# Performance work log

Measured on AMD Instinct MI355X. Metric: run time of the kernel, lower is better.

The kernel has to match this reference:

```python
import jax, jax.numpy as jnp
import numpy as np

B, N, E, H = 256, 256, 256, 512


def setup_inputs() -> dict:
    key = jax.random.key(0)
    ks = jax.random.split(key, 8)
    sH = 1.0 / np.sqrt(H)  # torch default init scale for LSTMCell / Linear fan_in
    sE = 1.0 / np.sqrt(E)
    return {
        "encoder_output": jax.random.normal(ks[0], (B, N, E), dtype=jnp.float32),
        "W_ih": jax.random.uniform(ks[1], (4 * H, E), jnp.float32, -sH, sH),
        "W_hh": jax.random.uniform(ks[2], (4 * H, H), jnp.float32, -sH, sH),
        "b_ih": jax.random.uniform(ks[3], (4 * H,), jnp.float32, -sH, sH),
        "b_hh": jax.random.uniform(ks[4], (4 * H,), jnp.float32, -sH, sH),
        "W_q": jax.random.uniform(ks[5], (H, H), jnp.float32, -sH, sH),
        "W_k": jax.random.uniform(ks[6], (H, E), jnp.float32, -sE, sE),
        "v": jax.random.uniform(ks[7], (H,), jnp.float32, -sH, sH),
        "max_steps": 256,
    }


def reference(encoder_output, W_ih, W_hh, b_ih, b_hh, W_q, W_k, v, max_steps):
    b, n, e = encoder_output.shape
    h_dim = W_hh.shape[1]
    # W_k(encoder_output) is loop-invariant -> hoist (same math as original)
    k_enc = jnp.einsum("bne,he->bnh", encoder_output, W_k)  # (B, N, H)
    keys = jax.random.split(jax.random.key(42), max_steps)
    batch_idx = jnp.arange(b)

    def step(carry, key):
        h, c, start, visited_mask = carry
        # torch LSTMCell: gates in i, f, g, o order
        gates = start @ W_ih.T + b_ih + h @ W_hh.T + b_hh  # (B, 4H)
        i, f, g, o = jnp.split(gates, 4, axis=-1)
        c = jax.nn.sigmoid(f) * c + jax.nn.sigmoid(i) * jnp.tanh(g)
        h = jax.nn.sigmoid(o) * jnp.tanh(c)
        q = h @ W_q.T  # (B, H)
        scores = jnp.einsum("bnh,h->bn", jnp.tanh(q[:, None, :] + k_enc), v)
        scores = scores - 1.0e6 * visited_mask
        probs = jax.nn.softmax(scores, axis=-1)
        # multinomial(probs, 1) == categorical over masked scores (logits)
        idx = jax.random.categorical(key, scores)  # (B,) int
        action_prob = jnp.take_along_axis(probs, idx[:, None], axis=1)[:, 0]
        visited_mask = visited_mask.at[batch_idx, idx].set(1.0)
        start = encoder_output[batch_idx, idx]  # (B, E)
        return (h, c, start, visited_mask), (idx, action_prob)

    init = (
        jnp.zeros((b, h_dim), jnp.float32),
        jnp.zeros((b, h_dim), jnp.float32),
        jnp.zeros((b, e), jnp.float32),
        jnp.zeros((b, n), jnp.float32),
    )
    _, (seq, action_probs) = jax.lax.scan(step, init, keys)
    action_sequence = seq.T  # (B, max_steps)
    logp_sum = jnp.sum(action_probs, axis=0)  # (B,) -- sums probs, as original does
    return action_sequence, logp_sum
```

## Files before the change

kernel.cpp:

```cpp
#include <hip/hip_runtime.h>
#include <cstdint>
#include <math.h>

typedef unsigned int u32;

#define BB 256
#define NN 256
#define EE 256
#define HH 512
#define G4 2048
#define KK 768
#define TT 256
#define NBLK 256
#define NTHR 1024

#define ALOADD(p)    __hip_atomic_load((p), __ATOMIC_RELAXED, __HIP_MEMORY_SCOPE_AGENT)
#define ASTORED(p,v) __hip_atomic_store((p), (v), __ATOMIC_RELAXED, __HIP_MEMORY_SCOPE_AGENT)
#define ALOADI(p)    __hip_atomic_load((p), __ATOMIC_RELAXED, __HIP_MEMORY_SCOPE_AGENT)
#define ASTOREI(p,v) __hip_atomic_store((p), (v), __ATOMIC_RELAXED, __HIP_MEMORY_SCOPE_AGENT)

__device__ __forceinline__ u32 rotl(u32 x, int d) { return (x << d) | (x >> (32 - d)); }

__device__ __forceinline__ void tf4(u32& x0, u32& x1, int r0, int r1, int r2, int r3) {
  x0 += x1; x1 = rotl(x1, r0); x1 ^= x0;
  x0 += x1; x1 = rotl(x1, r1); x1 ^= x0;
  x0 += x1; x1 = rotl(x1, r2); x1 ^= x0;
  x0 += x1; x1 = rotl(x1, r3); x1 ^= x0;
}

__device__ __forceinline__ void threefry2x32(u32 k0, u32 k1, u32 x0, u32 x1, u32& o0, u32& o1) {
  u32 k2 = k0 ^ k1 ^ 0x1BD11BDAu;
  x0 += k0; x1 += k1;
  tf4(x0, x1, 13, 15, 26, 6);  x0 += k1; x1 += k2 + 1u;
  tf4(x0, x1, 17, 29, 16, 24); x0 += k2; x1 += k0 + 2u;
  tf4(x0, x1, 13, 15, 26, 6);  x0 += k0; x1 += k1 + 3u;
  tf4(x0, x1, 17, 29, 16, 24); x0 += k1; x1 += k2 + 4u;
  tf4(x0, x1, 13, 15, 26, 6);  x0 += k2; x1 += k0 + 5u;
  o0 = x0; o1 = x1;
}

struct Args {
  const float *enc, *W_ih, *W_hh, *b_ih, *b_hh, *W_q, *W_k, *v;
  float *out;
  float *kT;
  float *Wc;
  float *WqT;
  double *bsum;
  u32 *keys;
  double *h0, *h1;
  double *c;
  double *q;
  int *idx;
  u32 *flags;
};

__device__ __forceinline__ void grid_barrier(u32* cnt, u32* gen) {
  __syncthreads();
  if (threadIdx.x == 0) {
    u32 g = __hip_atomic_load(gen, __ATOMIC_RELAXED, __HIP_MEMORY_SCOPE_AGENT);
    __threadfence();
    if (atomicAdd(cnt, 1u) == NBLK - 1u) {
      __hip_atomic_store(cnt, 0u, __ATOMIC_RELAXED, __HIP_MEMORY_SCOPE_AGENT);
      __threadfence();
      atomicAdd(gen, 1u);
    } else {
      while (__hip_atomic_load(gen, __ATOMIC_RELAXED, __HIP_MEMORY_SCOPE_AGENT) == g) {
        __builtin_amdgcn_s_sleep(2);
      }
    }
    __threadfence();
  }
  __syncthreads();
}

__device__ __forceinline__ void pod_signal(u32* ph, int pod, int me, u32 val) {
  asm volatile("s_waitcnt vmcnt(0)" ::: "memory");
  __syncthreads();
  if (threadIdx.x == 0) ASTOREI(&ph[pod * 32 + me], val);
}
__device__ __forceinline__ void pod_wait(u32* ph, int pod, u32 target) {
  const int t = threadIdx.x;
  if (t < 32) {
    while (ALOADI(&ph[pod * 32 + t]) < target) { __builtin_amdgcn_s_sleep(1); }
  }
  __syncthreads();
}

__global__ __launch_bounds__(NTHR) void mono_kernel(Args a) {
  const int blk = blockIdx.x;
  const int t = threadIdx.x;
  __shared__ alignas(16) unsigned char SMRAW[33344];
  __shared__ int visS[NN];
  __shared__ float vSp[HH];
  __shared__ double logpS;
  const int grp = blk >> 5;
  const int me  = blk & 31;
  const int jb = 4 * (blk & 7) + ((blk >> 3) & 3);
  u32* p1f = a.flags;
  u32* qf  = a.flags + 256;
  u32* p2f = a.flags + 512;

  {
    const int tid = blk * NTHR + t;
    const int tot = NBLK * NTHR;
    if (tid < BB * HH) { a.h0[tid] = 0.0; a.c[tid] = 0.0; }
    if (tid < BB) a.idx[tid] = -1;
    if (tid < 256) {
      u32 o0, o1;
      threefry2x32(0u, 42u, 0u, (u32)tid, o0, o1);
      a.keys[2 * tid] = o0; a.keys[2 * tid + 1] = o1;
    }
    if (tid < G4) a.bsum[tid] = (double)a.b_ih[tid] + (double)a.b_hh[tid];
    for (int i = tid; i < HH * HH; i += tot) {
      int h2 = i >> 9, h = i & 511;
      a.WqT[i] = a.W_q[h * HH + h2];
    }
    for (int i = tid; i < KK * G4; i += tot) {
      int k = i >> 11, col = i & 2047;
      int x16 = col >> 6, g = (col >> 4) & 3, w = col & 15;
      int j = g * HH + x16 * 16 + w;
      a.Wc[i] = (k < EE) ? a.W_ih[j * EE + k] : a.W_hh[j * HH + (k - EE)];
    }
    if (t < NN) visS[t] = 0;
    if (t < HH) vSp[t] = a.v[t];
    if (t == 0) logpS = 0.0;
  }
  {
    float (*encS)[65] = (float(*)[65])SMRAW;
    float (*wkS)[65]  = (float(*)[65])(SMRAW + 64 * 65 * 4);
    const int tn = t & 63, th = t >> 6;
    for (int tile = blk; tile < 8 * 4 * BB; tile += NBLK) {
      const int bx = tile & 7, by = (tile >> 3) & 3, b = tile >> 5;
      const int h0i = bx * 64, n0 = by * 64;
      double acc[4];
#pragma unroll
      for (int i = 0; i < 4; i++) acc[i] = 0.0;
      for (int ec = 0; ec < EE; ec += 64) {
        __syncthreads();
#pragma unroll
        for (int i = 0; i < 4; i++) {
          int idx = i * NTHR + t; int r = idx >> 6, cc = idx & 63;
          encS[r][cc] = a.enc[((size_t)b * NN + n0 + r) * EE + ec + cc];
          wkS[r][cc]  = a.W_k[(size_t)(h0i + r) * EE + ec + cc];
        }
        __syncthreads();
#pragma unroll 8
        for (int e = 0; e < 64; e++) {
          double ev = (double)encS[tn][e];
#pragma unroll
          for (int i = 0; i < 4; i++) acc[i] += (double)wkS[th * 4 + i][e] * ev;
        }
      }
#pragma unroll
      for (int i = 0; i < 4; i++)
        a.kT[((size_t)b * HH + h0i + th * 4 + i) * NN + n0 + tn] = (float)acc[i];
    }
  }
  grid_barrier(a.flags + 768, a.flags + 800);

  for (int step = 0; step < TT; step++) {
    double* hPrev = (step & 1) ? a.h1 : a.h0;
    double* hCur  = (step & 1) ? a.h0 : a.h1;
    const int b0 = grp * 32;

    if (step > 0) pod_wait(p2f, grp, (u32)step);

    {
      double (*aS)[33] = (double(*)[33])SMRAW;
      double (*bS)[66] = (double(*)[66])(SMRAW + 8448);
      int* idxP = (int*)(SMRAW + 25344);
      const int sr = t >> 5, scp = t & 31;
      const int bk = t >> 6, bc = t & 63;
      if (t < 32) idxP[t] = ALOADI(&a.idx[b0 + t]);
      __syncthreads();

      double aR; float bR0, bR1;
      {
        int iv = idxP[sr];
        aR = (iv >= 0) ? (double)a.enc[((size_t)(b0 + sr) * NN + iv) * EE + scp] : 0.0;
        bR0 = a.Wc[(size_t)(bk)      * G4 + jb * 64 + bc];
        bR1 = a.Wc[(size_t)(bk + 16) * G4 + jb * 64 + bc];
      }
      const int jc = t & 63, rg = t >> 6;
      double acc0, acc1, acc2, acc3;
      {
        double bv = a.bsum[(jc >> 4) * HH + jb * 16 + (jc & 15)];
        acc0 = bv; acc1 = bv; acc2 = bv; acc3 = bv;
      }
      for (int kc = 0; kc < KK; kc += 32) {
        aS[sr][scp] = aR;
        bS[bk][bc]      = (double)bR0;
        bS[bk + 16][bc] = (double)bR1;
        int kn = kc + 32;
        if (kn < KK) {
          if (kn < EE) {
            int iv = idxP[sr];
            aR = (iv >= 0) ? (double)a.enc[((size_t)(b0 + sr) * NN + iv) * EE + kn + scp] : 0.0;
          } else {
            aR = ALOADD(&hPrev[(size_t)(b0 + sr) * HH + (kn - EE) + scp]);
          }
          bR0 = a.Wc[(size_t)(kn + bk)      * G4 + jb * 64 + bc];
          bR1 = a.Wc[(size_t)(kn + bk + 16) * G4 + jb * 64 + bc];
        }
        __syncthreads();
        if (t < 512) {
#pragma unroll 8
          for (int kk = 0; kk < 32; kk++) {
            double bv = bS[kk][jc];
            acc0 += aS[rg * 4][kk]     * bv;
            acc1 += aS[rg * 4 + 1][kk] * bv;
            acc2 += aS[rg * 4 + 2][kk] * bv;
            acc3 += aS[rg * 4 + 3][kk] * bv;
          }
        }
        __syncthreads();
      }
      double (*gS)[66] = (double(*)[66])SMRAW;
      if (t < 512) {
        gS[rg * 4][jc]     = acc0;
        gS[rg * 4 + 1][jc] = acc1;
        gS[rg * 4 + 2][jc] = acc2;
        gS[rg * 4 + 3][jc] = acc3;
      }
      __syncthreads();
      if (t < 512) {
        const int b = t >> 4, w = t & 15;
        double ig = gS[b][w], fg = gS[b][16 + w], gv = gS[b][32 + w], og = gS[b][48 + w];
        double si = 1.0 / (1.0 + exp(-ig));
        double sf = 1.0 / (1.0 + exp(-fg));
        double so = 1.0 / (1.0 + exp(-og));
        size_t ci = (size_t)(b0 + b) * HH + jb * 16 + w;
        double cn = sf * a.c[ci] + si * tanh(gv);
        a.c[ci] = cn;
        ASTORED(&hCur[ci], so * tanh(cn));
      }
    }
    pod_signal(p1f, grp, me, (u32)(step + 1));
    pod_wait(p1f, grp, (u32)(step + 1));

    {
      double (*hS)[33] = (double(*)[33])SMRAW;
      float  (*wS)[17] = (float (*)[17])(SMRAW + 8448);
      const int sr = t >> 5, scp = t & 31;
      const int wk = t >> 4, wj = t & 15;
      const int j0 = jb * 16;
      double hR = ALOADD(&hCur[(size_t)(b0 + sr) * HH + scp]);
      float  wR = (t < 512) ? a.WqT[(size_t)wk * HH + j0 + wj] : 0.0f;
      const int bq = t >> 4, j = t & 15;
      double p0 = 0.0, p1 = 0.0, p2 = 0.0, p3 = 0.0;
      for (int kc = 0; kc < HH; kc += 32) {
        hS[sr][scp] = hR;
        if (t < 512) wS[wk][wj] = wR;
        int kn = kc + 32;
        if (kn < HH) {
          hR = ALOADD(&hCur[(size_t)(b0 + sr) * HH + kn + scp]);
          if (t < 512) wR = a.WqT[(size_t)(kn + wk) * HH + j0 + wj];
        }
        __syncthreads();
        if (t < 512) {
#pragma unroll 8
          for (int kk = 0; kk < 32; kk += 4) {
            p0 += hS[bq][kk]     * (double)wS[kk][j];
            p1 += hS[bq][kk + 1] * (double)wS[kk + 1][j];
            p2 += hS[bq][kk + 2] * (double)wS[kk + 2][j];
            p3 += hS[bq][kk + 3] * (double)wS[kk + 3][j];
          }
        }
        __syncthreads();
      }
      if (t < 512)
        ASTORED(&a.q[(size_t)(b0 + bq) * HH + j0 + j], (p0 + p1) + (p2 + p3));
    }
    pod_signal(qf, grp, me, (u32)(step + 1));
    pod_wait(qf, grp, (u32)(step + 1));

    {
      double* qS  = (double*)SMRAW;
      double* red = (double*)(SMRAW + 4096);
      double* sS  = (double*)(SMRAW + 12288);
      int*   redi = (int*)(SMRAW + 14336);
      int*   idxS = (int*)(SMRAW + 15360);
      const int b = blk;
      const int n = t & 255, quarter = t >> 8;
      if (t < 512) qS[t] = ALOADD(&a.q[(size_t)b * HH + t]);
      __syncthreads();

      const float* kp = a.kT + ((size_t)b * HH + quarter * 128) * NN + n;
      double a0 = 0.0, a1 = 0.0;
#pragma unroll 8
      for (int h = 0; h < 128; h += 2) {
        float k0 = kp[(size_t)h * NN];
        float k1 = kp[(size_t)(h + 1) * NN];
        int hh = quarter * 128 + h;
        a0 += (double)vSp[hh]     * (double)tanhf((float)(qS[hh]     + (double)k0));
        a1 += (double)vSp[hh + 1] * (double)tanhf((float)(qS[hh + 1] + (double)k1));
      }
      red[t] = a0 + a1;
      __syncthreads();

      if (t < 256) {
        double s = (red[t] + red[256 + t]) + (red[512 + t] + red[768 + t]);
        if (visS[t]) s -= 1.0e6;
        sS[t] = s;
      }
      __syncthreads();

      if (t < 256) {
        u32 fl = (u32)(b * 256 + t);
        u32 o0, o1;
        threefry2x32(a.keys[2 * step], a.keys[2 * step + 1], 0u, fl, o0, o1);
        u32 bits = o0 ^ o1;
        u32 fb = (bits >> 9) | 0x3F800000u;
        float uf = __uint_as_float(fb) - 1.0f;
        double u = (uf > 0.0f) ? (double)uf : (double)1.17549435e-38f;
        double gmb = -log(-log(u));
        red[t] = gmb + sS[t];
        redi[t] = t;
      }
      __syncthreads();
      for (int s2 = 128; s2 > 0; s2 >>= 1) {
        if (t < s2) {
          double v1 = red[t], v2 = red[t + s2];
          int i1 = redi[t], i2 = redi[t + s2];
          if (v2 > v1 || (v2 == v1 && i2 < i1)) { red[t] = v2; redi[t] = i2; }
        }
        __syncthreads();
      }
      if (t == 0) *idxS = redi[0];

      if (t < 256) red[t] = sS[t];
      __syncthreads();
      for (int s2 = 128; s2 > 0; s2 >>= 1) {
        if (t < s2) red[t] = fmax(red[t], red[t + s2]);
        __syncthreads();
      }
      double m = red[0];
      __syncthreads();
      if (t < 256) red[t] = exp(sS[t] - m);
      __syncthreads();
      for (int s2 = 128; s2 > 0; s2 >>= 1) {
        if (t < s2) red[t] += red[t + s2];
        __syncthreads();
      }
      if (t == 0) {
        int bi = *idxS;
        double p = exp(sS[bi] - m) / red[0];
        logpS += p;
        a.out[(size_t)b * TT + step] = (float)bi;
        visS[bi] = 1;
        ASTOREI(&a.idx[b], bi);
      }
    }
    pod_signal(p2f, grp, me, (u32)(step + 1));
  }

  if (t == 0) a.out[BB * TT + blk] = (float)logpS;
}

extern "C" void kernel_launch(void* const* d_in, const int* in_sizes, int n_in,
                              void* d_out, int out_size, void* d_ws, size_t ws_size,
                              hipStream_t stream) {
  char* ws = (char*)d_ws;
  Args a;
  a.enc  = (const float*)d_in[0];
  a.W_ih = (const float*)d_in[1];
  a.W_hh = (const float*)d_in[2];
  a.b_ih = (const float*)d_in[3];
  a.b_hh = (const float*)d_in[4];
  a.W_q  = (const float*)d_in[5];
  a.W_k  = (const float*)d_in[6];
  a.v    = (const float*)d_in[7];
  a.out  = (float*)d_out;

  a.kT    = (float*)(ws + 0);
  a.Wc    = (float*)(ws + 134217728);
  a.WqT   = (float*)(ws + 140509184);
  a.bsum  = (double*)(ws + 141557760);
  a.keys  = (u32*)(ws + 141574144);
  a.h0    = (double*)(ws + 141576192);
  a.h1    = (double*)(ws + 142624768);
  a.c     = (double*)(ws + 143673344);
  a.idx   = (int*)(ws + 144721920);
  a.flags = (u32*)(ws + 144723968);
  a.q     = (double*)(ws + 144728064);

  hipMemsetAsync((void*)a.flags, 0, 4096, stream);

  void* kargs[] = { &a };
  hipLaunchCooperativeKernel(reinterpret_cast<void*>(&mono_kernel),
                             dim3(NBLK), dim3(NTHR), kargs, 0, stream);
}
```

Before: 31.29 ms.

## Compute query projection per batch row locally and stage keys through double-buffered LDS

Each block now computes the full q row for its own batch element directly from h and WqT. Previously q was computed as a pod-distributed tile, written to global memory, and followed by a pod signal/wait barrier. Removing that inter-block barrier and the global q round trip cuts one synchronization point per step. Half the threads prefetch the k_enc slice into a double-buffered shared-memory tile with float4 loads while the other half compute q. The cost is redundant W_q reads per block (512x512 per block per step, with no tiling reuse) and higher LDS usage.

```diff
diff --git a/kernel.cpp b/kernel.cpp
--- a/kernel.cpp
+++ b/kernel.cpp
@@ -49,7 +49,6 @@
   u32 *keys;
   double *h0, *h1;
   double *c;
-  double *q;
   int *idx;
   u32 *flags;
 };
@@ -90,6 +89,7 @@
   const int blk = blockIdx.x;
   const int t = threadIdx.x;
   __shared__ alignas(16) unsigned char SMRAW[33344];
+  __shared__ float kS[2][32][260];
   __shared__ int visS[NN];
   __shared__ float vSp[HH];
   __shared__ double logpS;
@@ -97,7 +97,6 @@
   const int me  = blk & 31;
   const int jb = 4 * (blk & 7) + ((blk >> 3) & 3);
   u32* p1f = a.flags;
-  u32* qf  = a.flags + 256;
   u32* p2f = a.flags + 512;
 
   {
@@ -181,7 +180,7 @@
         bR0 = a.Wc[(size_t)(bk)      * G4 + jb * 64 + bc];
         bR1 = a.Wc[(size_t)(bk + 16) * G4 + jb * 64 + bc];
       }
-      const int jc = t & 63, rg = t >> 6;
+      const int jc = t & 63, rg2 = t >> 6;
       double acc0, acc1, acc2, acc3;
       {
         double bv = a.bsum[(jc >> 4) * HH + jb * 16 + (jc & 15)];
@@ -207,20 +206,20 @@
 #pragma unroll 8
           for (int kk = 0; kk < 32; kk++) {
             double bv = bS[kk][jc];
-            acc0 += aS[rg * 4][kk]     * bv;
-            acc1 += aS[rg * 4 + 1][kk] * bv;
-            acc2 += aS[rg * 4 + 2][kk] * bv;
-            acc3 += aS[rg * 4 + 3][kk] * bv;
+            acc0 += aS[rg2 * 4][kk]     * bv;
+            acc1 += aS[rg2 * 4 + 1][kk] * bv;
+            acc2 += aS[rg2 * 4 + 2][kk] * bv;
+            acc3 += aS[rg2 * 4 + 3][kk] * bv;
           }
         }
         __syncthreads();
       }
       double (*gS)[66] = (double(*)[66])SMRAW;
       if (t < 512) {
-        gS[rg * 4][jc]     = acc0;
-        gS[rg * 4 + 1][jc] = acc1;
-        gS[rg * 4 + 2][jc] = acc2;
-        gS[rg * 4 + 3][jc] = acc3;
+        gS[rg2 * 4][jc]     = acc0;
+        gS[rg2 * 4 + 1][jc] = acc1;
+        gS[rg2 * 4 + 2][jc] = acc2;
+        gS[rg2 * 4 + 3][jc] = acc3;
       }
       __syncthreads();
       if (t < 512) {
@@ -239,61 +238,72 @@
     pod_wait(p1f, grp, (u32)(step + 1));
 
     {
-      double (*hS)[33] = (double(*)[33])SMRAW;
-      float  (*wS)[17] = (float (*)[17])(SMRAW + 8448);
-      const int sr = t >> 5, scp = t & 31;
-      const int wk = t >> 4, wj = t & 15;
-      const int j0 = jb * 16;
-      double hR = ALOADD(&hCur[(size_t)(b0 + sr) * HH + scp]);
-      float  wR = (t < 512) ? a.WqT[(size_t)wk * HH + j0 + wj] : 0.0f;
-      const int bq = t >> 4, j = t & 15;
-      double p0 = 0.0, p1 = 0.0, p2 = 0.0, p3 = 0.0;
-      for (int kc = 0; kc < HH; kc += 32) {
-        hS[sr][scp] = hR;
-        if (t < 512) wS[wk][wj] = wR;
-        int kn = kc + 32;
-        if (kn < HH) {
-          hR = ALOADD(&hCur[(size_t)(b0 + sr) * HH + kn + scp]);
-          if (t < 512) wR = a.WqT[(size_t)(kn + wk) * HH + j0 + wj];
-        }
-        __syncthreads();
-        if (t < 512) {
+      double* hS  = (double*)SMRAW;
+      double* qS  = (double*)(SMRAW + 4096);
+      double* red = (double*)(SMRAW + 8192);
+      double* sS  = (double*)(SMRAW + 16384);
+      int*   redi = (int*)(SMRAW + 18432);
+      int*   idxS = (int*)(SMRAW + 19456);
+      const int b = blk;
+      const float* kTb = a.kT + (size_t)b * HH * NN;
+
+      const int u = t - 512;
+      const int lr = u >> 4, seg = (u & 15) * 16;
+      const int cq = lr >> 3, rq = lr & 7;
+
+      if (t < 512) hS[t] = ALOADD(&hCur[(size_t)b * HH + t]);
+      float4 rg[4];
+      if (t >= 512) {
+        const float* src = kTb + ((size_t)(cq * 128 + rq)) * NN + seg;
+#pragma unroll
+        for (int f = 0; f < 4; f++) rg[f] = *(const float4*)(src + 4 * f);
+      }
+      __syncthreads();
+
+      if (t < 512) {
+        const float* wp = a.WqT + t;
+        double p0 = 0.0, p1 = 0.0, p2 = 0.0, p3 = 0.0;
 #pragma unroll 8
-          for (int kk = 0; kk < 32; kk += 4) {
-            p0 += hS[bq][kk]     * (double)wS[kk][j];
-            p1 += hS[bq][kk + 1] * (double)wS[kk + 1][j];
-            p2 += hS[bq][kk + 2] * (double)wS[kk + 2][j];
-            p3 += hS[bq][kk + 3] * (double)wS[kk + 3][j];
+        for (int k = 0; k < HH; k += 4) {
+          p0 += hS[k]     * (double)wp[(size_t)k * HH];
+          p1 += hS[k + 1] * (double)wp[(size_t)(k + 1) * HH];
+          p2 += hS[k + 2] * (double)wp[(size_t)(k + 2) * HH];
+          p3 += hS[k + 3] * (double)wp[(size_t)(k + 3) * HH];
+        }
+        qS[t] = (p0 + p1) + (p2 + p3);
+      } else {
+#pragma unroll
+        for (int f = 0; f < 4; f++) *(float4*)&kS[0][lr][seg + 4 * f] = rg[f];
+        const float* src1 = kTb + ((size_t)(cq * 128 + 8 + rq)) * NN + seg;
+#pragma unroll
+        for (int f = 0; f < 4; f++) rg[f] = *(const float4*)(src1 + 4 * f);
+      }
+      __syncthreads();
+
+      const int n = t & 255, q = t >> 8;
+      double a0 = 0.0, a1 = 0.0;
+      for (int c = 0; c < 16; c++) {
+        const int cur = c & 1;
+        if (t >= 512) {
+          if (c + 1 < 16) {
+#pragma unroll
+            for (int f = 0; f < 4; f++) *(float4*)&kS[cur ^ 1][lr][seg + 4 * f] = rg[f];
           }
-        }
-        __syncthreads();
-      }
-      if (t < 512)
-        ASTORED(&a.q[(size_t)(b0 + bq) * HH + j0 + j], (p0 + p1) + (p2 + p3));
-    }
-    pod_signal(qf, grp, me, (u32)(step + 1));
-    pod_wait(qf, grp, (u32)(step + 1));
-
-    {
-      double* qS  = (double*)SMRAW;
-      double* red = (double*)(SMRAW + 4096);
-      double* sS  = (double*)(SMRAW + 12288);
-      int*   redi = (int*)(SMRAW + 14336);
-      int*   idxS = (int*)(SMRAW + 15360);
-      const int b = blk;
-      const int n = t & 255, quarter = t >> 8;
-      if (t < 512) qS[t] = ALOADD(&a.q[(size_t)b * HH + t]);
-      __syncthreads();
-
-      const float* kp = a.kT + ((size_t)b * HH + quarter * 128) * NN + n;
-      double a0 = 0.0, a1 = 0.0;
-#pragma unroll 8
-      for (int h = 0; h < 128; h += 2) {
-        float k0 = kp[(size_t)h * NN];
-        float k1 = kp[(size_t)(h + 1) * NN];
-        int hh = quarter * 128 + h;
-        a0 += (double)vSp[hh]     * (double)tanhf((float)(qS[hh]     + (double)k0));
-        a1 += (double)vSp[hh + 1] * (double)tanhf((float)(qS[hh + 1] + (double)k1));
+          if (c + 2 < 16) {
+            const float* srcn = kTb + ((size_t)(cq * 128 + (c + 2) * 8 + rq)) * NN + seg;
+#pragma unroll
+            for (int f = 0; f < 4; f++) rg[f] = *(const float4*)(srcn + 4 * f);
+          }
+        }
+#pragma unroll
+        for (int j = 0; j < 4; j++) {
+          float k0 = kS[cur][q * 8 + 2 * j][n];
+          float k1 = kS[cur][q * 8 + 2 * j + 1][n];
+          int hh = q * 128 + c * 8 + 2 * j;
+          a0 += (double)vSp[hh]     * (double)tanhf((float)(qS[hh]     + (double)k0));
+          a1 += (double)vSp[hh + 1] * (double)tanhf((float)(qS[hh + 1] + (double)k1));
+        }
+        __syncthreads();
       }
       red[t] = a0 + a1;
       __syncthreads();
@@ -312,8 +322,8 @@
         u32 bits = o0 ^ o1;
         u32 fb = (bits >> 9) | 0x3F800000u;
         float uf = __uint_as_float(fb) - 1.0f;
-        double u = (uf > 0.0f) ? (double)uf : (double)1.17549435e-38f;
-        double gmb = -log(-log(u));
+        double uu = (uf > 0.0f) ? (double)uf : (double)1.17549435e-38f;
+        double gmb = -log(-log(uu));
         red[t] = gmb + sS[t];
         redi[t] = t;
       }
@@ -382,7 +392,6 @@
   a.c     = (double*)(ws + 143673344);
   a.idx   = (int*)(ws + 144721920);
   a.flags = (u32*)(ws + 144723968);
-  a.q     = (double*)(ws + 144728064);
 
   hipMemsetAsync((void*)a.flags, 0, 4096, stream);
 
```

Result: slower. 67.10 ms (+114.4%).
